# Optimization experiments

Hardware: AMD Instinct MI355X
Metric: run time of the kernel (lower is better)

The kernel has to match this reference:

```python
import jax, jax.numpy as jnp
import numpy as np

SCORE_THR = 0.3
NMS_IOU = 0.3
TOPK = 100          # fixed candidate budget replacing dynamic boolean masking
IMAGE_SHAPE = (512, 512)  # (H, W); letterbox_image=False so scale is direct


def pool_nms(heat):
    # 3x3 max-pool peak-NMS: keep only local maxima
    pooled = jax.lax.reduce_window(heat, -jnp.inf, jax.lax.max,
                                   (1, 1, 3, 3), (1, 1, 1, 1), 'SAME')
    return heat * (pooled == heat).astype(heat.dtype)


def setup_inputs() -> dict:
    key = jax.random.key(0)
    k1, k2, k3 = jax.random.split(key, 3)
    hm = jax.random.uniform(k1, (32, 80, 128, 128), dtype=jnp.float32)
    wh = jax.random.uniform(k2, (32, 2, 128, 128), dtype=jnp.float32) * 8.0
    offset = jax.random.uniform(k3, (32, 2, 128, 128), dtype=jnp.float32)
    return {"hm": hm, "wh": wh, "offset": offset}


def reference(hm, wh, offset):
    B, C, H, W = hm.shape
    HW = H * W
    heat = pool_nms(hm)
    heat = heat.transpose(0, 2, 3, 1).reshape(B, HW, C)       # [B,HW,C]
    whf = wh.transpose(0, 2, 3, 1).reshape(B, HW, 2)           # [B,HW,2]
    off = offset.transpose(0, 2, 3, 1).reshape(B, HW, 2)       # [B,HW,2]

    conf = heat.max(-1)                                        # [B,HW]
    cls = jnp.argmax(heat, -1)                                 # [B,HW]

    idx = jnp.arange(HW)
    xv = (idx % W).astype(hm.dtype)
    yv = (idx // W).astype(hm.dtype)
    cx = xv[None, :] + off[..., 0]
    cy = yv[None, :] + off[..., 1]
    bw = whf[..., 0]
    bh = whf[..., 1]
    # normalized xyxy boxes, as in decode_bbox
    boxes = jnp.stack([(cx - bw / 2) / W, (cy - bh / 2) / H,
                       (cx + bw / 2) / W, (cy + bh / 2) / H], -1)  # [B,HW,4]

    scores = jnp.where(conf > SCORE_THR, conf, 0.0)
    top_s, top_i = jax.lax.top_k(scores, TOPK)                 # sorted desc
    tb = jnp.take_along_axis(boxes, top_i[..., None], axis=1)  # [B,K,4]
    tc = jnp.take_along_axis(cls, top_i, axis=1)               # [B,K]
    valid = top_s > SCORE_THR                                  # [B,K]

    # per-class greedy NMS on score-sorted candidates (fixed size K)
    area = (tb[..., 2] - tb[..., 0]) * (tb[..., 3] - tb[..., 1])
    lt = jnp.maximum(tb[:, :, None, :2], tb[:, None, :, :2])
    rb = jnp.minimum(tb[:, :, None, 2:], tb[:, None, :, 2:])
    whi = jnp.clip(rb - lt, 0.0)
    inter = whi[..., 0] * whi[..., 1]
    iou = inter / (area[:, :, None] + area[:, None, :] - inter + 1e-9)
    supmat = (iou > NMS_IOU) & (tc[:, :, None] == tc[:, None, :])  # [B,K,K]

    j = jnp.arange(TOPK)

    def body(i, keep):
        alive_i = jnp.take(keep, i, axis=1)[:, None]           # [B,1]
        sup = jnp.take(supmat, i, axis=1) & (j[None, :] > i) & alive_i
        return keep & ~sup

    keep = jax.lax.fori_loop(0, TOPK, body, valid)             # [B,K]

    # centernet_correct_boxes with letterbox_image=False: scale to image size
    ih, iw = IMAGE_SHAPE
    cxy = (tb[..., :2] + tb[..., 2:]) / 2
    cwh = tb[..., 2:] - tb[..., :2]
    mins = cxy - cwh / 2
    maxs = cxy + cwh / 2
    scale = jnp.array([iw, ih, iw, ih], hm.dtype)
    bimg = jnp.concatenate([mins, maxs], -1) * scale           # [B,K,4]

    dets = jnp.concatenate([bimg, top_s[..., None],
                            tc[..., None].astype(hm.dtype)], -1)  # [B,K,6]
    return jnp.where(keep[..., None], dets, 0.0)
```

## Files before the change

### kernel.cpp

```cpp
#include <hip/hip_runtime.h>
#include <hip/hip_bf16.h>
#include <stdint.h>

#define HH 128
#define WW 128
#define CC 80
#define HW (HH * WW)
#define BB 32
#define TOPK 100
#define NTHREADS 256
#define SCORE_THR 0.3f
#define NMS_IOU 0.3f
#define BUF 512
#define MINT 0x3E99999Bu

__global__ __launch_bounds__(NTHREADS, 2)
void heat_reduce(const float* __restrict__ hm,
                 float* __restrict__ conf_out,
                 unsigned char* __restrict__ cls_out) {
    const int stripe = blockIdx.x & 15;
    const int b      = blockIdx.x >> 4;
    const int tid    = threadIdx.x;
    const int c31    = tid & 31;
    const int r      = tid >> 5;
    const int x4     = c31 << 2;
    const int y      = stripe * 8 + r;
    const int yM     = (y > 0) ? y - 1 : 0;
    const int yP     = (y < HH - 1) ? y + 1 : y;
    const bool leftClamp  = (c31 == 0);
    const bool rightClamp = (c31 == 31);

    const float* bbase = hm + (size_t)b * CC * HW;
    const size_t o0 = (size_t)yM * WW + x4;
    const size_t o1 = (size_t)y  * WW + x4;
    const size_t o2 = (size_t)yP * WW + x4;

    float conf[4] = {0.f, 0.f, 0.f, 0.f};
    int   cls[4]  = {0, 0, 0, 0};

    auto rowmax = [&](float4 a, float rm[4]) {
        float le = __shfl_up(a.w, 1, 64);
        float re = __shfl_down(a.x, 1, 64);
        if (leftClamp)  le = a.x;
        if (rightClamp) re = a.w;
        rm[0] = fmaxf(fmaxf(le,  a.x), a.y);
        rm[1] = fmaxf(fmaxf(a.x, a.y), a.z);
        rm[2] = fmaxf(fmaxf(a.y, a.z), a.w);
        rm[3] = fmaxf(fmaxf(a.z, a.w), re);
    };

#pragma unroll 8
    for (int c = 0; c < CC; ++c) {
        const float* p = bbase + (size_t)c * HW;
        float4 a0 = *(const float4*)(p + o0);
        float4 a1 = *(const float4*)(p + o1);
        float4 a2 = *(const float4*)(p + o2);
        float rm0[4], rm1[4], rm2[4];
        rowmax(a0, rm0);
        rowmax(a1, rm1);
        rowmax(a2, rm2);
        float ctr[4] = {a1.x, a1.y, a1.z, a1.w};
#pragma unroll
        for (int i = 0; i < 4; ++i) {
            float pool = fmaxf(fmaxf(rm0[i], rm1[i]), rm2[i]);
            float heat = (ctr[i] == pool) ? ctr[i] : 0.0f;
            if (heat > conf[i]) { conf[i] = heat; cls[i] = c; }
        }
    }

    size_t idx = (size_t)b * HW + (size_t)y * WW + x4;
    *(float4*)&conf_out[idx] =
        make_float4(conf[0], conf[1], conf[2], conf[3]);
    uchar4 cv = make_uchar4((unsigned char)cls[0], (unsigned char)cls[1],
                            (unsigned char)cls[2], (unsigned char)cls[3]);
    *(uchar4*)&cls_out[idx] = cv;
}

__global__ __launch_bounds__(NTHREADS, 1)
void select_nms(const float* __restrict__ conf_m,
                const unsigned char* __restrict__ cls_m,
                const float* __restrict__ wh,
                const float* __restrict__ offset,
                float* __restrict__ out) {
    const int b    = blockIdx.x;
    const int tid  = threadIdx.x;
    const int lane = tid & 63;
    const int wid  = tid >> 6;
    constexpr int VALS = HW / NTHREADS;

    __shared__ int wsum[4];
    __shared__ unsigned int sCnt;
    __shared__ unsigned long long keys[BUF];

    unsigned u[VALS];
#pragma unroll
    for (int k = 0; k < VALS; ++k) {
        int i = k * NTHREADS + tid;
        float best = conf_m[(size_t)b * HW + i];
        u[k] = (best > SCORE_THR) ? __float_as_uint(best) : 0u;
    }

    auto blockCount = [&](unsigned T) -> int {
        int c = 0;
#pragma unroll
        for (int k = 0; k < VALS; ++k) c += (u[k] >= T);
        for (int o = 32; o > 0; o >>= 1) c += __shfl_down(c, o, 64);
        if (lane == 0) wsum[wid] = c;
        __syncthreads();
        int tot = wsum[0] + wsum[1] + wsum[2] + wsum[3];
        __syncthreads();
        return tot;
    };

    unsigned V;
    {
        unsigned lo = MINT, hi = 0x3F800001u;
        int cl = blockCount(lo);
        if (cl < TOPK) {
            V = lo;
        } else {
            while (hi - lo > 1u) {
                unsigned mid = lo + ((hi - lo) >> 1);
                if (blockCount(mid) >= TOPK) lo = mid; else hi = mid;
            }
            V = lo;
        }
    }

    if (tid == 0) sCnt = 0;
    for (int i = tid; i < BUF; i += NTHREADS) keys[i] = 0ull;
    __syncthreads();
#pragma unroll
    for (int k = 0; k < VALS; ++k) {
        if (u[k] >= V) {
            int i = k * NTHREADS + tid;
            unsigned pos = atomicAdd(&sCnt, 1u);
            if (pos < BUF)
                keys[pos] = ((unsigned long long)u[k] << 32) |
                            (unsigned)(HW - 1 - i);
        }
    }
    __syncthreads();
    int cnt = (int)sCnt;
    if (cnt > BUF) cnt = BUF;

    int n = 1;
    while (n < cnt) n <<= 1;
    for (int k = 2; k <= n; k <<= 1) {
        for (int j = k >> 1; j > 0; j >>= 1) {
            for (int i = tid; i < n; i += NTHREADS) {
                int p = i ^ j;
                if (p > i) {
                    unsigned long long a = keys[i], bb2 = keys[p];
                    bool asc_seg = ((i & k) != 0);
                    bool sw = asc_seg ? (a > bb2) : (a < bb2);
                    if (sw) { keys[i] = bb2; keys[p] = a; }
                }
            }
            __syncthreads();
        }
    }

    __shared__ float bx[TOPK][4];
    __shared__ float barea[TOPK];
    __shared__ float bsc[TOPK];
    __shared__ int   bcls[TOPK];
    __shared__ int   keep[TOPK];

    if (tid < TOPK) {
        unsigned long long kk = keys[tid];
        float sc = __uint_as_float((unsigned)(kk >> 32));
        int   i  = HW - 1 - (int)(kk & 0xFFFFFFFFull);
        int   y  = (i >> 7) & 127;
        int   x  = i & 127;
        int   bc = (int)cls_m[(size_t)b * HW + i];

        size_t base = (size_t)b * 2 * HW + (size_t)y * WW + x;
        float ox = offset[base];
        float oy = offset[base + HW];
        float w  = wh[base];
        float hh = wh[base + HW];
        float cx = (float)x + ox;
        float cy = (float)y + oy;
        float x1 = (cx - w  * 0.5f) * (1.0f / 128.0f);
        float y1 = (cy - hh * 0.5f) * (1.0f / 128.0f);
        float x2 = (cx + w  * 0.5f) * (1.0f / 128.0f);
        float y2 = (cy + hh * 0.5f) * (1.0f / 128.0f);
        bx[tid][0] = x1; bx[tid][1] = y1; bx[tid][2] = x2; bx[tid][3] = y2;
        barea[tid] = (x2 - x1) * (y2 - y1);
        bsc[tid]   = sc;
        bcls[tid]  = bc;
        keep[tid]  = (sc > SCORE_THR) ? 1 : 0;
    }
    __syncthreads();

    if (tid < 64) {
        const int A  = tid;
        const int Bq = tid + 64;
        float aX0 = bx[A][0], aY0 = bx[A][1], aX1 = bx[A][2], aY1 = bx[A][3];
        float aAr = barea[A]; int aC = bcls[A]; int kA = keep[A];
        float bX0 = 0, bY0 = 0, bX1 = 0, bY1 = 0, bAr = 0;
        int   bC = -1, kB = 0;
        if (Bq < TOPK) {
            bX0 = bx[Bq][0]; bY0 = bx[Bq][1]; bX1 = bx[Bq][2]; bY1 = bx[Bq][3];
            bAr = barea[Bq]; bC = bcls[Bq]; kB = keep[Bq];
        }
        for (int i = 0; i < TOPK; ++i) {
            int kv    = (i < 64) ? kA : kB;
            int alive = __shfl(kv, i & 63, 64);
            if (alive) {
                float iX0 = bx[i][0], iY0 = bx[i][1];
                float iX1 = bx[i][2], iY1 = bx[i][3];
                float iAr = barea[i]; int iC = bcls[i];
                if (A > i && aC == iC) {
                    float lx = fmaxf(aX0, iX0), ly = fmaxf(aY0, iY0);
                    float rx = fminf(aX1, iX1), ry = fminf(aY1, iY1);
                    float iw = fmaxf(rx - lx, 0.f), ih = fmaxf(ry - ly, 0.f);
                    float inter = iw * ih;
                    float iou = inter / (aAr + iAr - inter + 1e-9f);
                    if (iou > NMS_IOU) kA = 0;
                }
                if (Bq > i && Bq < TOPK && bC == iC) {
                    float lx = fmaxf(bX0, iX0), ly = fmaxf(bY0, iY0);
                    float rx = fminf(bX1, iX1), ry = fminf(bY1, iY1);
                    float iw = fmaxf(rx - lx, 0.f), ih = fmaxf(ry - ly, 0.f);
                    float inter = iw * ih;
                    float iou = inter / (bAr + iAr - inter + 1e-9f);
                    if (iou > NMS_IOU) kB = 0;
                }
            }
        }
        keep[A] = kA;
        if (Bq < TOPK) keep[Bq] = kB;
    }
    __syncthreads();

    for (int t = tid; t < TOPK * 6; t += NTHREADS) {
        int j = t / 6, comp = t - j * 6;
        float v = 0.0f;
        if (keep[j]) {
            if (comp < 4)       v = bx[j][comp] * 512.0f;
            else if (comp == 4) v = bsc[j];
            else                v = (float)bcls[j];
        }
        out[(size_t)b * (TOPK * 6) + t] = v;
    }
}

extern "C" void kernel_launch(void* const* d_in, const int* in_sizes, int n_in,
                              void* d_out, int out_size, void* d_ws, size_t ws_size,
                              hipStream_t stream) {
    const float* hm     = (const float*)d_in[0];
    const float* wh     = (const float*)d_in[1];
    const float* offset = (const float*)d_in[2];
    float* out = (float*)d_out;

    float* confm = (float*)d_ws;
    unsigned char* clsm = (unsigned char*)d_ws + (size_t)BB * HW * 4;

    heat_reduce<<<BB * 16, NTHREADS, 0, stream>>>(hm, confm, clsm);
    select_nms<<<BB, NTHREADS, 0, stream>>>(confm, clsm, wh, offset, out);
}
```

Baseline: 326.6 us.

## Split heat reduction over four class groups and merge partials in select kernel

The heatmap pool/argmax kernel now splits the 80 classes into four groups, launching four times as many blocks, each writing partial conf/class planes. The select kernel takes the max of the four partial planes and recovers the class, preferring the earliest group on ties. The heat loop also prefetches the next channel's rows in software, and the occupancy hint rises to 8. The aim is more parallelism and latency hiding for the memory-bound pass over hm, at the cost of 4x partial workspace traffic and extra reads in select_nms.

```diff
diff --git a/kernel.cpp b/kernel.cpp
--- a/kernel.cpp
+++ b/kernel.cpp
@@ -12,14 +12,18 @@
 #define SCORE_THR 0.3f
 #define NMS_IOU 0.3f
 #define BUF 512
+#define GG 4
+#define PLANE ((size_t)BB * HW)
 #define MINT 0x3E99999Bu
 
-__global__ __launch_bounds__(NTHREADS, 2)
+__global__ __launch_bounds__(NTHREADS, 8)
 void heat_reduce(const float* __restrict__ hm,
-                 float* __restrict__ conf_out,
-                 unsigned char* __restrict__ cls_out) {
+                 float* __restrict__ conf_part,
+                 unsigned char* __restrict__ cls_part) {
+    constexpr int CPG = CC / GG;
     const int stripe = blockIdx.x & 15;
-    const int b      = blockIdx.x >> 4;
+    const int g      = (blockIdx.x >> 4) & 3;
+    const int b      = blockIdx.x >> 6;
     const int tid    = threadIdx.x;
     const int c31    = tid & 31;
     const int r      = tid >> 5;
@@ -29,14 +33,14 @@
     const int yP     = (y < HH - 1) ? y + 1 : y;
     const bool leftClamp  = (c31 == 0);
     const bool rightClamp = (c31 == 31);
-
-    const float* bbase = hm + (size_t)b * CC * HW;
-    const size_t o0 = (size_t)yM * WW + x4;
-    const size_t o1 = (size_t)y  * WW + x4;
-    const size_t o2 = (size_t)yP * WW + x4;
+    const int c0     = g * CPG;
+
+    const float* p0 = hm + (size_t)(b * CC + c0) * HW + (size_t)yM * WW + x4;
+    const float* p1 = hm + (size_t)(b * CC + c0) * HW + (size_t)y  * WW + x4;
+    const float* p2 = hm + (size_t)(b * CC + c0) * HW + (size_t)yP * WW + x4;
 
     float conf[4] = {0.f, 0.f, 0.f, 0.f};
-    int   cls[4]  = {0, 0, 0, 0};
+    int   cls[4]  = {c0, c0, c0, c0};
 
     auto rowmax = [&](float4 a, float rm[4]) {
         float le = __shfl_up(a.w, 1, 64);
@@ -49,17 +53,24 @@
         rm[3] = fmaxf(fmaxf(a.z, a.w), re);
     };
 
-#pragma unroll 8
-    for (int c = 0; c < CC; ++c) {
-        const float* p = bbase + (size_t)c * HW;
-        float4 a0 = *(const float4*)(p + o0);
-        float4 a1 = *(const float4*)(p + o1);
-        float4 a2 = *(const float4*)(p + o2);
+    float4 n0 = *(const float4*)p0;
+    float4 n1 = *(const float4*)p1;
+    float4 n2 = *(const float4*)p2;
+
+    for (int cc = 0; cc < CPG; ++cc) {
+        float4 a0 = n0, a1 = n1, a2 = n2;
+        if (cc + 1 < CPG) {
+            p0 += HW; p1 += HW; p2 += HW;
+            n0 = *(const float4*)p0;
+            n1 = *(const float4*)p1;
+            n2 = *(const float4*)p2;
+        }
         float rm0[4], rm1[4], rm2[4];
         rowmax(a0, rm0);
         rowmax(a1, rm1);
         rowmax(a2, rm2);
         float ctr[4] = {a1.x, a1.y, a1.z, a1.w};
+        const int c = c0 + cc;
 #pragma unroll
         for (int i = 0; i < 4; ++i) {
             float pool = fmaxf(fmaxf(rm0[i], rm1[i]), rm2[i]);
@@ -68,17 +79,17 @@
         }
     }
 
-    size_t idx = (size_t)b * HW + (size_t)y * WW + x4;
-    *(float4*)&conf_out[idx] =
-        make_float4(conf[0], conf[1], conf[2], conf[3]);
-    uchar4 cv = make_uchar4((unsigned char)cls[0], (unsigned char)cls[1],
-                            (unsigned char)cls[2], (unsigned char)cls[3]);
-    *(uchar4*)&cls_out[idx] = cv;
+    size_t idx = (size_t)g * PLANE + (size_t)b * HW + (size_t)y * WW + x4;
+    *(float4*)&conf_part[idx] = make_float4(conf[0], conf[1], conf[2], conf[3]);
+    *(uchar4*)&cls_part[idx]  = make_uchar4((unsigned char)cls[0],
+                                            (unsigned char)cls[1],
+                                            (unsigned char)cls[2],
+                                            (unsigned char)cls[3]);
 }
 
 __global__ __launch_bounds__(NTHREADS, 1)
-void select_nms(const float* __restrict__ conf_m,
-                const unsigned char* __restrict__ cls_m,
+void select_nms(const float* __restrict__ conf_part,
+                const unsigned char* __restrict__ cls_part,
                 const float* __restrict__ wh,
                 const float* __restrict__ offset,
                 float* __restrict__ out) {
@@ -95,8 +106,12 @@
     unsigned u[VALS];
 #pragma unroll
     for (int k = 0; k < VALS; ++k) {
-        int i = k * NTHREADS + tid;
-        float best = conf_m[(size_t)b * HW + i];
+        size_t base = (size_t)b * HW + (k * NTHREADS + tid);
+        float s0 = conf_part[base];
+        float s1 = conf_part[PLANE + base];
+        float s2 = conf_part[2 * PLANE + base];
+        float s3 = conf_part[3 * PLANE + base];
+        float best = fmaxf(fmaxf(s0, s1), fmaxf(s2, s3));
         u[k] = (best > SCORE_THR) ? __float_as_uint(best) : 0u;
     }
 
@@ -173,7 +188,14 @@
         int   i  = HW - 1 - (int)(kk & 0xFFFFFFFFull);
         int   y  = (i >> 7) & 127;
         int   x  = i & 127;
-        int   bc = (int)cls_m[(size_t)b * HW + i];
+        size_t base0 = (size_t)b * HW + i;
+        float bcf = conf_part[base0];
+        int   bc  = (int)cls_part[base0];
+#pragma unroll
+        for (int gg = 1; gg < GG; ++gg) {
+            float cf = conf_part[gg * PLANE + base0];
+            if (cf > bcf) { bcf = cf; bc = (int)cls_part[gg * PLANE + base0]; }
+        }
 
         size_t base = (size_t)b * 2 * HW + (size_t)y * WW + x;
         float ox = offset[base];
@@ -255,9 +277,9 @@
     const float* offset = (const float*)d_in[2];
     float* out = (float*)d_out;
 
-    float* confm = (float*)d_ws;
-    unsigned char* clsm = (unsigned char*)d_ws + (size_t)BB * HW * 4;
-
-    heat_reduce<<<BB * 16, NTHREADS, 0, stream>>>(hm, confm, clsm);
-    select_nms<<<BB, NTHREADS, 0, stream>>>(confm, clsm, wh, offset, out);
+    float* confp = (float*)d_ws;
+    unsigned char* clsp = (unsigned char*)d_ws + GG * PLANE * 4;
+
+    heat_reduce<<<BB * GG * 16, NTHREADS, 0, stream>>>(hm, confp, clsp);
+    select_nms<<<BB, NTHREADS, 0, stream>>>(confp, clsp, wh, offset, out);
 }
```

Result: faster. 292.5 us (-10.4%).
